# Kernel tuning notes

Hardware: AMD Instinct MI355X
Metric: run time of the kernel (lower is better)

Reference implementation:

```python
import jax, jax.numpy as jnp
import numpy as np

NUM_HEADS = 16
D_MODEL = 1024
DEPTH = D_MODEL // NUM_HEADS
THRESHOLD = 0.1
BATCH = 2
SEQ = 2048


def setup_inputs() -> dict:
    key = jax.random.key(0)
    ks = jax.random.split(key, 9)
    w_scale = 1.0 / np.sqrt(D_MODEL)
    Q = jax.random.normal(ks[0], (BATCH, SEQ, D_MODEL), dtype=jnp.float32)
    T = jax.random.normal(ks[1], (BATCH, SEQ, D_MODEL), dtype=jnp.float32)
    V = jax.random.normal(ks[2], (BATCH, SEQ, D_MODEL), dtype=jnp.float32)
    Wq = jax.random.normal(ks[3], (NUM_HEADS, D_MODEL, DEPTH), dtype=jnp.float32) * w_scale
    Wk = jax.random.normal(ks[4], (NUM_HEADS, D_MODEL, DEPTH), dtype=jnp.float32) * w_scale
    Wv = jax.random.normal(ks[5], (NUM_HEADS, D_MODEL, DEPTH), dtype=jnp.float32) * w_scale
    Wo = jax.random.normal(ks[6], (D_MODEL, D_MODEL), dtype=jnp.float32) * w_scale
    bq = jnp.zeros((NUM_HEADS, DEPTH), dtype=jnp.float32)
    bk = jnp.zeros((NUM_HEADS, DEPTH), dtype=jnp.float32)
    bv = jnp.zeros((NUM_HEADS, DEPTH), dtype=jnp.float32)
    bo = jnp.zeros((D_MODEL,), dtype=jnp.float32)
    return {"Q": Q, "T": T, "V": V, "Wq": Wq, "bq": bq, "Wk": Wk, "bk": bk,
            "Wv": Wv, "bv": bv, "Wo": Wo, "bo": bo}


def reference(Q, T, V, Wq, bq, Wk, bk, Wv, bv, Wo, bo):
    # Per-head projections (stacked over heads): [B,S,D] x [H,D,E] -> [B,H,S,E]
    q = jnp.einsum('bsd,hde->bhse', Q, Wq) + bq[None, :, None, :]
    k = jnp.einsum('bsd,hde->bhse', T, Wk) + bk[None, :, None, :]
    v = jnp.einsum('bsd,hde->bhse', V, Wv) + bv[None, :, None, :]

    # Raw scores (NOT pre-scaled): [B,H,S,S]
    scores = jnp.einsum('bhqe,bhke->bhqk', q, k)
    # tf.where(A>thr, A, -2**32 * cast(A>thr)) -> failing entries become 0
    scores = jnp.where(scores > THRESHOLD, scores, jnp.zeros((), scores.dtype))
    # M = 1 - lower_band(ones): +1 on strictly upper-triangular entries
    seq = scores.shape[-1]
    upper = jnp.triu(jnp.ones((seq, seq), dtype=scores.dtype), k=1)
    scores = (scores + upper) / jnp.sqrt(jnp.asarray(DEPTH, scores.dtype))

    attn = jax.nn.softmax(scores, axis=-1)
    out = jnp.einsum('bhqk,bhke->bhqe', attn, v)  # [B,H,S,E]
    B, H, S, E = out.shape
    concat = out.transpose(0, 2, 1, 3).reshape(B, S, H * E)  # [B,S,D]
    return concat @ Wo + bo
```

## Files before the change

### kernel.cpp

```cpp
#include <hip/hip_runtime.h>
#include <stdint.h>


typedef __attribute__((ext_vector_type(8))) short bf16x8;
typedef __attribute__((ext_vector_type(4))) float f32x4;

#define DEVFN static __device__ __forceinline__

static constexpr int S_ = 2048;
static constexpr int H_ = 16;

DEVFN unsigned short f2bf(float x) {
  union { float f; uint32_t u; } v; v.f = x;
  const uint32_t r = v.u + 0x7fffu + ((v.u >> 16) & 1u);
  return (unsigned short)(r >> 16);
}

DEVFN f32x4 fzero() { f32x4 v = {0.f, 0.f, 0.f, 0.f}; return v; }

DEVFN void gld_lds16(const void* g, void* lds) {
  __builtin_amdgcn_global_load_lds(
      (const __attribute__((address_space(1))) void*)g,
      (__attribute__((address_space(3))) void*)lds, 16, 0, 0);
}

__global__ void prep_weights(const float* __restrict__ Wq, const float* __restrict__ Wk,
                             const float* __restrict__ Wv, const float* __restrict__ Wo,
                             unsigned short* __restrict__ dstBase) {
  const int z = blockIdx.z;
  const float* src = (z == 0) ? Wq : (z == 1) ? Wk : (z == 2) ? Wv : Wo;
  unsigned short* dst = dstBase + (size_t)z * (1024u * 1024u);
  const int idx = blockIdx.x * 256 + threadIdx.x;
  const int c = idx & 1023;
  const int d0 = (idx >> 10) << 3;
  unsigned short hv[8];
#pragma unroll
  for (int t = 0; t < 8; ++t) {
    const int d = d0 + t;
    const float v = (z < 3) ? src[(size_t)((c >> 6) * 1024 + d) * 64 + (c & 63)]
                            : src[(size_t)d * 1024 + c];
    hv[t] = f2bf(v);
  }
  *(uint4*)(dst + (size_t)c * 1024 + d0) = *(const uint4*)hv;
}

__global__ void convert_a(const float* __restrict__ Qm, const float* __restrict__ Tm,
                          const float* __restrict__ Vm, unsigned short* __restrict__ aq,
                          unsigned short* __restrict__ at2, unsigned short* __restrict__ av) {
  const int z = blockIdx.z;
  const float* s = (z == 0) ? Qm : (z == 1) ? Tm : Vm;
  unsigned short* d = (z == 0) ? aq : (z == 1) ? at2 : av;
  const size_t i = ((size_t)blockIdx.x * 256 + threadIdx.x) * 8;
  const float4 f0 = *(const float4*)(s + i);
  const float4 f1 = *(const float4*)(s + i + 4);
  uint32_t d0, d1, d2, d3;
  asm("v_cvt_pk_bf16_f32 %0, %1, %2" : "=v"(d0) : "v"(f0.x), "v"(f0.y));
  asm("v_cvt_pk_bf16_f32 %0, %1, %2" : "=v"(d1) : "v"(f0.z), "v"(f0.w));
  asm("v_cvt_pk_bf16_f32 %0, %1, %2" : "=v"(d2) : "v"(f1.x), "v"(f1.y));
  asm("v_cvt_pk_bf16_f32 %0, %1, %2" : "=v"(d3) : "v"(f1.z), "v"(f1.w));
  uint4 o; o.x = d0; o.y = d1; o.z = d2; o.w = d3;
  *(uint4*)(d + i) = o;
}

__global__ __launch_bounds__(256, 4)
void proj_gemm(const unsigned short* __restrict__ Aq,
               const unsigned short* __restrict__ At2,
               const unsigned short* __restrict__ Av,
               const unsigned short* __restrict__ Wt,
               const float* __restrict__ bq, const float* __restrict__ bk,
               const float* __restrict__ bv, unsigned short* __restrict__ qb,
               unsigned short* __restrict__ kb, unsigned short* __restrict__ vtb) {
  __shared__ unsigned short At[2][128 * 32];
  __shared__ unsigned short Bt[2][128 * 32];

  const int tid = threadIdx.x;
  const int lane = tid & 63;
  const int w = tid >> 6;
  const int g = lane >> 4, c = lane & 15;
  const int wm = w >> 1, wn = w & 1;

  const int m0 = blockIdx.x * 128;
  const int proj = blockIdx.y >> 3;
  const int n0 = (blockIdx.y & 7) * 128;

  const unsigned short* Abf = (proj == 0) ? Aq : (proj == 1) ? At2 : Av;
  const unsigned short* W = Wt + (size_t)proj * (1024u * 1024u);

  f32x4 acc[4][4];
#pragma unroll
  for (int i = 0; i < 4; ++i)
#pragma unroll
    for (int j = 0; j < 4; ++j) acc[i][j] = fzero();

  const int srow = lane >> 2;
  const int sch = lane & 3;

  auto stage = [&](int kt, int buf) {
#pragma unroll
    for (int u = 0; u < 2; ++u) {
      const int row = u * 64 + w * 16 + srow;
      const int ch = sch ^ ((row >> 1) & 3);
      gld_lds16(Abf + (size_t)(m0 + row) * 1024 + kt * 32 + ch * 8,
                &At[buf][(u * 64 + w * 16) * 32]);
      gld_lds16(W + (size_t)(n0 + row) * 1024 + kt * 32 + ch * 8,
                &Bt[buf][(u * 64 + w * 16) * 32]);
    }
  };

  stage(0, 0);
  __syncthreads();

  for (int kt = 0; kt < 32; ++kt) {
    const int buf = kt & 1;
    if (kt < 31) stage(kt + 1, buf ^ 1);

    bf16x8 af[4], bfr[4];
#pragma unroll
    for (int mi = 0; mi < 4; ++mi) {
      const int row = wm * 64 + mi * 16 + c;
      af[mi] = *(const bf16x8*)&At[buf][row * 32 + ((g ^ ((row >> 1) & 3))) * 8];
    }
#pragma unroll
    for (int ni = 0; ni < 4; ++ni) {
      const int row = wn * 64 + ni * 16 + c;
      bfr[ni] = *(const bf16x8*)&Bt[buf][row * 32 + ((g ^ ((row >> 1) & 3))) * 8];
    }
#pragma unroll
    for (int mi = 0; mi < 4; ++mi)
#pragma unroll
      for (int ni = 0; ni < 4; ++ni)
        acc[mi][ni] = __builtin_amdgcn_mfma_f32_16x16x32_bf16(af[mi], bfr[ni],
                                                              acc[mi][ni], 0, 0, 0);
    __syncthreads();
  }

  const float* bias = (proj == 0) ? bq : (proj == 1) ? bk : bv;
#pragma unroll
  for (int ni = 0; ni < 4; ++ni) {
    const int colb = n0 + wn * 64 + ni * 16 + c;
    const float bc = bias[colb];
    const int hh = colb >> 6, e = colb & 63;
#pragma unroll
    for (int mi = 0; mi < 4; ++mi) {
#pragma unroll
      for (int r = 0; r < 4; ++r) {
        const int row = m0 + wm * 64 + mi * 16 + g * 4 + r;
        const int bb = row >> 11, s = row & 2047;
        const float val = acc[mi][ni][r] + bc;
        if (proj < 2) {
          unsigned short* d = (proj == 0) ? qb : kb;
          d[(((size_t)(bb * H_ + hh)) * S_ + s) * 64 + e] = f2bf(val);
        } else {
          vtb[(((size_t)(bb * H_ + hh)) * 64 + e) * S_ + s] = f2bf(val);
        }
      }
    }
  }
}

__global__ __launch_bounds__(256, 4)
void attn_kernel(const unsigned short* __restrict__ qb,
                 const unsigned short* __restrict__ kb,
                 const unsigned short* __restrict__ vtb,
                 unsigned short* __restrict__ att) {
  __shared__ unsigned short Kt[2][64 * 64];
  __shared__ unsigned short Vt[2][64 * 64];
  __shared__ unsigned short Pt[4][16 * 64];

  const int tid = threadIdx.x;
  const int lane = tid & 63;
  const int w = tid >> 6;
  const int g = lane >> 4, c = lane & 15;

  const int orig = blockIdx.x;
  const int logical = ((orig & 7) << 7) | (orig >> 3);
  const int qblk = logical & 31;
  const int bh = logical >> 5;
  const int hh = bh & 15, bz = bh >> 4;

  const int q0w = qblk * 64 + w * 16;
  const unsigned short* qh = qb + (size_t)bh * S_ * 64;
  const unsigned short* kh = kb + (size_t)bh * S_ * 64;
  const unsigned short* vh = vtb + (size_t)bh * 64 * S_;

  bf16x8 aq[2];
#pragma unroll
  for (int t = 0; t < 2; ++t)
    aq[t] = *(const bf16x8*)&qh[(size_t)(q0w + c) * 64 + t * 32 + g * 8];

  f32x4 O[4];
#pragma unroll
  for (int ne = 0; ne < 4; ++ne) O[ne] = fzero();
  float l_lane = 0.f;

  constexpr float L2E = 1.4426950408889634f;
  const float S2 = 0.125f * L2E;
  const float B2 = 0.125f * L2E;
  const int iq = q0w + c;

  const int srow = w * 8 + (lane >> 3);
  const int sch = lane & 7;

  {
#pragma unroll
    for (int u = 0; u < 2; ++u) {
      const int row = u * 32 + srow;
      gld_lds16(kh + (size_t)row * 64 + (sch ^ (row & 7)) * 8,
                &Kt[0][(u * 32 + w * 8) * 64]);
      gld_lds16(vh + (size_t)row * S_ + (sch ^ (row & 7)) * 8,
                &Vt[0][(u * 32 + w * 8) * 64]);
    }
  }
  __syncthreads();

  for (int jt = 0; jt < 32; ++jt) {
    const int cur = jt & 1;
    const int j0 = jt * 64;

    if (jt < 31) {
      const int jn = j0 + 64;
#pragma unroll
      for (int u = 0; u < 2; ++u) {
        const int row = u * 32 + srow;
        gld_lds16(kh + (size_t)(jn + row) * 64 + (sch ^ (row & 7)) * 8,
                  &Kt[cur ^ 1][(u * 32 + w * 8) * 64]);
        gld_lds16(vh + (size_t)row * S_ + jn + (sch ^ (row & 7)) * 8,
                  &Vt[cur ^ 1][(u * 32 + w * 8) * 64]);
      }
    }

    f32x4 sa[4];
#pragma unroll
    for (int mi = 0; mi < 4; ++mi) sa[mi] = fzero();
    __builtin_amdgcn_s_setprio(1);
#pragma unroll
    for (int ks = 0; ks < 2; ++ks) {
#pragma unroll
      for (int mi = 0; mi < 4; ++mi) {
        const int row = mi * 16 + c;
        const bf16x8 ka =
            *(const bf16x8*)&Kt[cur][row * 64 + ((ks * 4 + g) ^ (row & 7)) * 8];
        sa[mi] = __builtin_amdgcn_mfma_f32_16x16x32_bf16(ka, aq[ks], sa[mi], 0, 0, 0);
      }
    }
    __builtin_amdgcn_s_setprio(0);

    float pe[16];
    const bool allUp = (j0 >= q0w + 16);
    const bool noneUp = (j0 + 63 <= q0w);
    if (allUp || noneUp) {
      const float bb = allUp ? B2 : 0.f;
#pragma unroll
      for (int i = 0; i < 16; ++i) {
        const float v = sa[i >> 2][i & 3];
        const float arg = (v > 0.1f) ? __builtin_fmaf(v, S2, bb) : bb;
        pe[i] = __builtin_amdgcn_exp2f(arg);
      }
    } else {
#pragma unroll
      for (int mi = 0; mi < 4; ++mi)
#pragma unroll
        for (int r = 0; r < 4; ++r) {
          const float v = sa[mi][r];
          const float bb = (j0 + mi * 16 + g * 4 + r > iq) ? B2 : 0.f;
          const float arg = (v > 0.1f) ? __builtin_fmaf(v, S2, bb) : bb;
          pe[mi * 4 + r] = __builtin_amdgcn_exp2f(arg);
        }
    }

    {
      float s01 = pe[0] + pe[1], s23 = pe[2] + pe[3];
      float s45 = pe[4] + pe[5], s67 = pe[6] + pe[7];
      float s89 = pe[8] + pe[9], sab = pe[10] + pe[11];
      float scd = pe[12] + pe[13], sef = pe[14] + pe[15];
      l_lane += ((s01 + s23) + (s45 + s67)) + ((s89 + sab) + (scd + sef));
    }

#pragma unroll
    for (int mi = 0; mi < 4; ++mi) {
      uint2 d;
      asm("v_cvt_pk_bf16_f32 %0, %1, %2"
          : "=v"(d.x) : "v"(pe[mi * 4 + 0]), "v"(pe[mi * 4 + 1]));
      asm("v_cvt_pk_bf16_f32 %0, %1, %2"
          : "=v"(d.y) : "v"(pe[mi * 4 + 2]), "v"(pe[mi * 4 + 3]));
      const int pc = (2 * mi + (g >> 1)) ^ (c & 7);
      *(uint2*)&Pt[w][c * 64 + pc * 8 + (g & 1) * 4] = d;
    }
    asm volatile("s_waitcnt lgkmcnt(0)" ::: "memory");
    __builtin_amdgcn_sched_barrier(0);

    __builtin_amdgcn_s_setprio(1);
#pragma unroll
    for (int ks = 0; ks < 2; ++ks) {
      const bf16x8 pa =
          *(const bf16x8*)&Pt[w][c * 64 + (((ks * 4 + g) ^ (c & 7))) * 8];
#pragma unroll
      for (int ne = 0; ne < 4; ++ne) {
        const int e = ne * 16 + c;
        const bf16x8 bv8 =
            *(const bf16x8*)&Vt[cur][e * 64 + ((ks * 4 + g) ^ (e & 7)) * 8];
        O[ne] = __builtin_amdgcn_mfma_f32_16x16x32_bf16(pa, bv8, O[ne], 0, 0, 0);
      }
    }
    __builtin_amdgcn_s_setprio(0);
    __syncthreads();
  }

  float l = l_lane;
  l += __shfl_xor(l, 16);
  l += __shfl_xor(l, 32);
  const float invl = 1.f / l;
  const int base = (lane >> 2) & 12;
  float il[4];
#pragma unroll
  for (int r = 0; r < 4; ++r) il[r] = __shfl(invl, base + r);
#pragma unroll
  for (int r = 0; r < 4; ++r) {
    const int qg = q0w + g * 4 + r;
    const size_t ro = ((size_t)(bz * S_ + qg)) * 1024 + hh * 64;
#pragma unroll
    for (int ne = 0; ne < 4; ++ne)
      att[ro + ne * 16 + c] = f2bf(O[ne][r] * il[r]);
  }
}

__global__ __launch_bounds__(256, 3)
void out_gemm(const unsigned short* __restrict__ att,
              const unsigned short* __restrict__ WoT,
              const float* __restrict__ bo, float* __restrict__ outp) {
  __shared__ unsigned short At[2][128 * 32];
  __shared__ unsigned short Bt[2][128 * 32];

  const int tid = threadIdx.x;
  const int lane = tid & 63;
  const int w = tid >> 6;
  const int g = lane >> 4, c = lane & 15;
  const int wm = w >> 1, wn = w & 1;
  const int m0 = blockIdx.x * 128;
  const int n0 = blockIdx.y * 128;

  f32x4 acc[4][4];
#pragma unroll
  for (int i = 0; i < 4; ++i)
#pragma unroll
    for (int j = 0; j < 4; ++j) acc[i][j] = fzero();

  const int srow = lane >> 2;
  const int sch = lane & 3;

  auto stage = [&](int kt, int buf) {
#pragma unroll
    for (int u = 0; u < 2; ++u) {
      const int row = u * 64 + w * 16 + srow;
      const int ch = sch ^ ((row >> 1) & 3);
      gld_lds16(att + (size_t)(m0 + row) * 1024 + kt * 32 + ch * 8,
                &At[buf][(u * 64 + w * 16) * 32]);
      gld_lds16(WoT + (size_t)(n0 + row) * 1024 + kt * 32 + ch * 8,
                &Bt[buf][(u * 64 + w * 16) * 32]);
    }
  };

  stage(0, 0);
  __syncthreads();

  for (int kt = 0; kt < 32; ++kt) {
    const int buf = kt & 1;
    if (kt < 31) stage(kt + 1, buf ^ 1);

    bf16x8 af[4], bfr[4];
#pragma unroll
    for (int mi = 0; mi < 4; ++mi) {
      const int row = wm * 64 + mi * 16 + c;
      af[mi] = *(const bf16x8*)&At[buf][row * 32 + ((g ^ ((row >> 1) & 3))) * 8];
    }
#pragma unroll
    for (int ni = 0; ni < 4; ++ni) {
      const int row = wn * 64 + ni * 16 + c;
      bfr[ni] = *(const bf16x8*)&Bt[buf][row * 32 + ((g ^ ((row >> 1) & 3))) * 8];
    }
#pragma unroll
    for (int mi = 0; mi < 4; ++mi)
#pragma unroll
      for (int ni = 0; ni < 4; ++ni)
        acc[mi][ni] = __builtin_amdgcn_mfma_f32_16x16x32_bf16(af[mi], bfr[ni],
                                                              acc[mi][ni], 0, 0, 0);
    __syncthreads();
  }

#pragma unroll
  for (int ni = 0; ni < 4; ++ni) {
    const int colb = n0 + wn * 64 + ni * 16 + c;
    const float bc = bo[colb];
#pragma unroll
    for (int mi = 0; mi < 4; ++mi)
#pragma unroll
      for (int r = 0; r < 4; ++r) {
        const int row = m0 + wm * 64 + mi * 16 + g * 4 + r;
        outp[(size_t)row * 1024 + colb] = acc[mi][ni][r] + bc;
      }
  }
}

extern "C" void kernel_launch(void* const* d_in, const int* in_sizes, int n_in,
                              void* d_out, int out_size, void* d_ws, size_t ws_size,
                              hipStream_t stream) {
  const float* Q  = (const float*)d_in[0];
  const float* T  = (const float*)d_in[1];
  const float* V  = (const float*)d_in[2];
  const float* Wq = (const float*)d_in[3];
  const float* bq = (const float*)d_in[4];
  const float* Wk = (const float*)d_in[5];
  const float* bk = (const float*)d_in[6];
  const float* Wv = (const float*)d_in[7];
  const float* bv = (const float*)d_in[8];
  const float* Wo = (const float*)d_in[9];
  const float* bo = (const float*)d_in[10];

  const size_t MB = 1024ull * 1024ull;
  if (ws_size < 40 * MB) return;

  uint8_t* ws = (uint8_t*)d_ws;
  unsigned short* Wt  = (unsigned short*)(ws);
  unsigned short* qb  = (unsigned short*)(ws + 8 * MB);
  unsigned short* kb  = (unsigned short*)(ws + 16 * MB);
  unsigned short* vtb = (unsigned short*)(ws + 24 * MB);
  unsigned short* attb = (unsigned short*)(ws + 32 * MB);

  unsigned short* aQ = (unsigned short*)d_out;
  unsigned short* aT = aQ + 4ull * 1024ull * 1024ull;
  unsigned short* aV = attb;

  prep_weights<<<dim3(512, 1, 4), 256, 0, stream>>>(Wq, Wk, Wv, Wo, Wt);
  convert_a<<<dim3(2048, 1, 3), 256, 0, stream>>>(Q, T, V, aQ, aT, aV);
  proj_gemm<<<dim3(32, 24), 256, 0, stream>>>(aQ, aT, aV, Wt, bq, bk, bv,
                                              qb, kb, vtb);
  attn_kernel<<<dim3(1024), 256, 0, stream>>>(qb, kb, vtb, attb);
  out_gemm<<<dim3(32, 8), 256, 0, stream>>>(attb, Wt + 3ull * 1024ull * 1024ull,
                                            bo, (float*)d_out);
}
```

Before: 146.4 us.

## Compute softmax denominator via MFMA with ones, precompute LDS offsets, unroll tile loop

The attention kernel now computes the softmax row sum with an extra MFMA against a ones vector on the bf16 probabilities. This replaces the per-lane float accumulation and the shuffle reduction, so the denominator now comes from bf16-rounded values, matching what the PV product uses. LDS read/write offsets and global source pointers are precomputed outside the loop, and the tile loop is manually unrolled by two so the buffer index is a compile-time constant. The V projection epilogue also packs four bf16 values into one 8-byte store, replacing scalar strided stores.

Measured after the change: 138.1 us. -5.6%, faster.

```diff
diff --git a/kernel.cpp b/kernel.cpp
--- a/kernel.cpp
+++ b/kernel.cpp
@@ -135,24 +135,38 @@
   }
 
   const float* bias = (proj == 0) ? bq : (proj == 1) ? bk : bv;
-#pragma unroll
-  for (int ni = 0; ni < 4; ++ni) {
-    const int colb = n0 + wn * 64 + ni * 16 + c;
-    const float bc = bias[colb];
-    const int hh = colb >> 6, e = colb & 63;
-#pragma unroll
-    for (int mi = 0; mi < 4; ++mi) {
-#pragma unroll
-      for (int r = 0; r < 4; ++r) {
-        const int row = m0 + wm * 64 + mi * 16 + g * 4 + r;
-        const int bb = row >> 11, s = row & 2047;
-        const float val = acc[mi][ni][r] + bc;
-        if (proj < 2) {
-          unsigned short* d = (proj == 0) ? qb : kb;
-          d[(((size_t)(bb * H_ + hh)) * S_ + s) * 64 + e] = f2bf(val);
-        } else {
-          vtb[(((size_t)(bb * H_ + hh)) * 64 + e) * S_ + s] = f2bf(val);
+  if (proj < 2) {
+    unsigned short* dptr = (proj == 0) ? qb : kb;
+#pragma unroll
+    for (int ni = 0; ni < 4; ++ni) {
+      const int colb = n0 + wn * 64 + ni * 16 + c;
+      const float bc = bias[colb];
+      const int hh = colb >> 6, e = colb & 63;
+#pragma unroll
+      for (int mi = 0; mi < 4; ++mi)
+#pragma unroll
+        for (int r = 0; r < 4; ++r) {
+          const int row = m0 + wm * 64 + mi * 16 + g * 4 + r;
+          const int bb = row >> 11, s = row & 2047;
+          dptr[(((size_t)(bb * H_ + hh)) * S_ + s) * 64 + e] = f2bf(acc[mi][ni][r] + bc);
         }
+    }
+  } else {
+#pragma unroll
+    for (int ni = 0; ni < 4; ++ni) {
+      const int colb = n0 + wn * 64 + ni * 16 + c;
+      const float bc = bias[colb];
+      const int hh = colb >> 6, e = colb & 63;
+#pragma unroll
+      for (int mi = 0; mi < 4; ++mi) {
+        const int rowb = m0 + wm * 64 + mi * 16 + g * 4;
+        const int bb = rowb >> 11, s0 = rowb & 2047;
+        const float v0 = acc[mi][ni][0] + bc, v1 = acc[mi][ni][1] + bc;
+        const float v2 = acc[mi][ni][2] + bc, v3 = acc[mi][ni][3] + bc;
+        uint2 pk;
+        asm("v_cvt_pk_bf16_f32 %0, %1, %2" : "=v"(pk.x) : "v"(v0), "v"(v1));
+        asm("v_cvt_pk_bf16_f32 %0, %1, %2" : "=v"(pk.y) : "v"(v2), "v"(v3));
+        *(uint2*)&vtb[(((size_t)(bb * H_ + hh)) * 64 + e) * S_ + s0] = pk;
       }
     }
   }
@@ -188,139 +202,142 @@
   for (int t = 0; t < 2; ++t)
     aq[t] = *(const bf16x8*)&qh[(size_t)(q0w + c) * 64 + t * 32 + g * 8];
 
+  bf16x8 onesB;
+#pragma unroll
+  for (int i = 0; i < 8; ++i) onesB[i] = (short)0x3F80;
+
   f32x4 O[4];
+  f32x4 accL;
 #pragma unroll
   for (int ne = 0; ne < 4; ++ne) O[ne] = fzero();
-  float l_lane = 0.f;
+  accL = fzero();
 
   constexpr float L2E = 1.4426950408889634f;
   const float S2 = 0.125f * L2E;
   const float B2 = 0.125f * L2E;
   const int iq = q0w + c;
 
+  int kaOff[2][4], bvOff[2][4], paOff[2], pwOff[4];
+#pragma unroll
+  for (int ks = 0; ks < 2; ++ks) {
+#pragma unroll
+    for (int mi = 0; mi < 4; ++mi) {
+      const int row = mi * 16 + c;
+      kaOff[ks][mi] = 2 * (row * 64 + ((ks * 4 + g) ^ (row & 7)) * 8);
+    }
+#pragma unroll
+    for (int ne = 0; ne < 4; ++ne) {
+      const int e = ne * 16 + c;
+      bvOff[ks][ne] = 2 * (e * 64 + ((ks * 4 + g) ^ (e & 7)) * 8);
+    }
+    paOff[ks] = 2 * (c * 64 + ((ks * 4 + g) ^ (c & 7)) * 8);
+  }
+#pragma unroll
+  for (int mi = 0; mi < 4; ++mi)
+    pwOff[mi] = 2 * (c * 64 + ((2 * mi + (g >> 1)) ^ (c & 7)) * 8 + (g & 1) * 4);
+
   const int srow = w * 8 + (lane >> 3);
-  const int sch = lane & 7;
+  const int sch = (lane & 7) ^ (srow & 7);
+  const unsigned short* kS0 = kh + (size_t)srow * 64 + sch * 8;
+  const unsigned short* kS1 = kh + (size_t)(32 + srow) * 64 + sch * 8;
+  const unsigned short* vS0 = vh + (size_t)srow * S_ + sch * 8;
+  const unsigned short* vS1 = vh + (size_t)(32 + srow) * S_ + sch * 8;
 
   {
-#pragma unroll
-    for (int u = 0; u < 2; ++u) {
-      const int row = u * 32 + srow;
-      gld_lds16(kh + (size_t)row * 64 + (sch ^ (row & 7)) * 8,
-                &Kt[0][(u * 32 + w * 8) * 64]);
-      gld_lds16(vh + (size_t)row * S_ + (sch ^ (row & 7)) * 8,
-                &Vt[0][(u * 32 + w * 8) * 64]);
-    }
+    gld_lds16(kS0, &Kt[0][(w * 8) * 64]);
+    gld_lds16(kS1, &Kt[0][(32 + w * 8) * 64]);
+    gld_lds16(vS0, &Vt[0][(w * 8) * 64]);
+    gld_lds16(vS1, &Vt[0][(32 + w * 8) * 64]);
   }
   __syncthreads();
 
-  for (int jt = 0; jt < 32; ++jt) {
-    const int cur = jt & 1;
-    const int j0 = jt * 64;
-
-    if (jt < 31) {
-      const int jn = j0 + 64;
-#pragma unroll
-      for (int u = 0; u < 2; ++u) {
-        const int row = u * 32 + srow;
-        gld_lds16(kh + (size_t)(jn + row) * 64 + (sch ^ (row & 7)) * 8,
-                  &Kt[cur ^ 1][(u * 32 + w * 8) * 64]);
-        gld_lds16(vh + (size_t)row * S_ + jn + (sch ^ (row & 7)) * 8,
-                  &Vt[cur ^ 1][(u * 32 + w * 8) * 64]);
-      }
-    }
-
-    f32x4 sa[4];
-#pragma unroll
-    for (int mi = 0; mi < 4; ++mi) sa[mi] = fzero();
-    __builtin_amdgcn_s_setprio(1);
-#pragma unroll
-    for (int ks = 0; ks < 2; ++ks) {
-#pragma unroll
-      for (int mi = 0; mi < 4; ++mi) {
-        const int row = mi * 16 + c;
-        const bf16x8 ka =
-            *(const bf16x8*)&Kt[cur][row * 64 + ((ks * 4 + g) ^ (row & 7)) * 8];
-        sa[mi] = __builtin_amdgcn_mfma_f32_16x16x32_bf16(ka, aq[ks], sa[mi], 0, 0, 0);
-      }
-    }
-    __builtin_amdgcn_s_setprio(0);
-
-    float pe[16];
-    const bool allUp = (j0 >= q0w + 16);
-    const bool noneUp = (j0 + 63 <= q0w);
-    if (allUp || noneUp) {
-      const float bb = allUp ? B2 : 0.f;
-#pragma unroll
-      for (int i = 0; i < 16; ++i) {
-        const float v = sa[i >> 2][i & 3];
-        const float arg = (v > 0.1f) ? __builtin_fmaf(v, S2, bb) : bb;
-        pe[i] = __builtin_amdgcn_exp2f(arg);
-      }
-    } else {
-#pragma unroll
-      for (int mi = 0; mi < 4; ++mi)
-#pragma unroll
-        for (int r = 0; r < 4; ++r) {
-          const float v = sa[mi][r];
-          const float bb = (j0 + mi * 16 + g * 4 + r > iq) ? B2 : 0.f;
-          const float arg = (v > 0.1f) ? __builtin_fmaf(v, S2, bb) : bb;
-          pe[mi * 4 + r] = __builtin_amdgcn_exp2f(arg);
-        }
-    }
-
-    {
-      float s01 = pe[0] + pe[1], s23 = pe[2] + pe[3];
-      float s45 = pe[4] + pe[5], s67 = pe[6] + pe[7];
-      float s89 = pe[8] + pe[9], sab = pe[10] + pe[11];
-      float scd = pe[12] + pe[13], sef = pe[14] + pe[15];
-      l_lane += ((s01 + s23) + (s45 + s67)) + ((s89 + sab) + (scd + sef));
-    }
-
-#pragma unroll
-    for (int mi = 0; mi < 4; ++mi) {
-      uint2 d;
-      asm("v_cvt_pk_bf16_f32 %0, %1, %2"
-          : "=v"(d.x) : "v"(pe[mi * 4 + 0]), "v"(pe[mi * 4 + 1]));
-      asm("v_cvt_pk_bf16_f32 %0, %1, %2"
-          : "=v"(d.y) : "v"(pe[mi * 4 + 2]), "v"(pe[mi * 4 + 3]));
-      const int pc = (2 * mi + (g >> 1)) ^ (c & 7);
-      *(uint2*)&Pt[w][c * 64 + pc * 8 + (g & 1) * 4] = d;
-    }
-    asm volatile("s_waitcnt lgkmcnt(0)" ::: "memory");
-    __builtin_amdgcn_sched_barrier(0);
-
-    __builtin_amdgcn_s_setprio(1);
-#pragma unroll
-    for (int ks = 0; ks < 2; ++ks) {
-      const bf16x8 pa =
-          *(const bf16x8*)&Pt[w][c * 64 + (((ks * 4 + g) ^ (c & 7))) * 8];
-#pragma unroll
-      for (int ne = 0; ne < 4; ++ne) {
-        const int e = ne * 16 + c;
-        const bf16x8 bv8 =
-            *(const bf16x8*)&Vt[cur][e * 64 + ((ks * 4 + g) ^ (e & 7)) * 8];
-        O[ne] = __builtin_amdgcn_mfma_f32_16x16x32_bf16(pa, bv8, O[ne], 0, 0, 0);
-      }
-    }
-    __builtin_amdgcn_s_setprio(0);
-    __syncthreads();
-  }
-
-  float l = l_lane;
-  l += __shfl_xor(l, 16);
-  l += __shfl_xor(l, 32);
-  const float invl = 1.f / l;
-  const int base = (lane >> 2) & 12;
-  float il[4];
-#pragma unroll
-  for (int r = 0; r < 4; ++r) il[r] = __shfl(invl, base + r);
+#define ATTN_BODY(JT, CUR)                                                     \
+  do {                                                                         \
+    const int j0 = (JT) * 64;                                                  \
+    if ((JT) < 31) {             \
+      gld_lds16(kS0 + 4096, &Kt[CUR ^ 1][(w * 8) * 64]);                       \
+      gld_lds16(kS1 + 4096, &Kt[CUR ^ 1][(32 + w * 8) * 64]);                  \
+      gld_lds16(vS0 + 64, &Vt[CUR ^ 1][(w * 8) * 64]);                         \
+      gld_lds16(vS1 + 64, &Vt[CUR ^ 1][(32 + w * 8) * 64]);                    \
+      kS0 += 4096; kS1 += 4096; vS0 += 64; vS1 += 64;                          \
+    }                                                                          \
+    f32x4 sa[4];                                                               \
+    _Pragma("unroll")                                                          \
+    for (int mi = 0; mi < 4; ++mi) sa[mi] = fzero();                           \
+    __builtin_amdgcn_s_setprio(1);                                             \
+    _Pragma("unroll")                                                          \
+    for (int ks = 0; ks < 2; ++ks)                                             \
+      _Pragma("unroll")                                                        \
+      for (int mi = 0; mi < 4; ++mi) {                                         \
+        const bf16x8 ka =                                                      \
+            *(const bf16x8*)((const char*)&Kt[CUR][0] + kaOff[ks][mi]);        \
+        sa[mi] = __builtin_amdgcn_mfma_f32_16x16x32_bf16(ka, aq[ks], sa[mi],   \
+                                                         0, 0, 0);             \
+      }                                                                        \
+    __builtin_amdgcn_s_setprio(0);                                             \
+    const bool allUp = (j0 >= q0w + 16);                                       \
+    const bool noneUp = (j0 + 63 <= q0w);                                      \
+    _Pragma("unroll")                                                          \
+    for (int mi = 0; mi < 4; ++mi) {                                           \
+      float pv[4];                                                             \
+      if (allUp || noneUp) {                                                   \
+        const float bb = allUp ? B2 : 0.f;                                     \
+        _Pragma("unroll")                                                      \
+        for (int r = 0; r < 4; ++r) {                                          \
+          const float v = sa[mi][r];                                           \
+          pv[r] = __builtin_amdgcn_exp2f((v > 0.1f)                            \
+                                             ? __builtin_fmaf(v, S2, bb)      \
+                                             : bb);                            \
+        }                                                                      \
+      } else {                                                                 \
+        _Pragma("unroll")                                                      \
+        for (int r = 0; r < 4; ++r) {                                          \
+          const float v = sa[mi][r];                                           \
+          const float bb = (j0 + mi * 16 + g * 4 + r > iq) ? B2 : 0.f;         \
+          pv[r] = __builtin_amdgcn_exp2f((v > 0.1f)                            \
+                                             ? __builtin_fmaf(v, S2, bb)      \
+                                             : bb);                           \
+        }                                                                      \
+      }                                                                        \
+      uint2 d;                                                                 \
+      asm("v_cvt_pk_bf16_f32 %0, %1, %2" : "=v"(d.x) : "v"(pv[0]), "v"(pv[1]));\
+      asm("v_cvt_pk_bf16_f32 %0, %1, %2" : "=v"(d.y) : "v"(pv[2]), "v"(pv[3]));\
+      *(uint2*)((char*)&Pt[w][0] + pwOff[mi]) = d;                             \
+    }                                                                          \
+    asm volatile("s_waitcnt lgkmcnt(0)" ::: "memory");                         \
+    __builtin_amdgcn_sched_barrier(0);                                         \
+    __builtin_amdgcn_s_setprio(1);                                             \
+    _Pragma("unroll")                                                          \
+    for (int ks = 0; ks < 2; ++ks) {                                           \
+      const bf16x8 pa =                                                        \
+          *(const bf16x8*)((const char*)&Pt[w][0] + paOff[ks]);                \
+      accL = __builtin_amdgcn_mfma_f32_16x16x32_bf16(pa, onesB, accL, 0, 0, 0);\
+      _Pragma("unroll")                                                        \
+      for (int ne = 0; ne < 4; ++ne) {                                         \
+        const bf16x8 bv8 =                                                     \
+            *(const bf16x8*)((const char*)&Vt[CUR][0] + bvOff[ks][ne]);        \
+        O[ne] = __builtin_amdgcn_mfma_f32_16x16x32_bf16(pa, bv8, O[ne],        \
+                                                        0, 0, 0);              \
+      }                                                                        \
+    }                                                                          \
+    __builtin_amdgcn_s_setprio(0);                                             \
+    __syncthreads();                                                           \
+  } while (0)
+
+  for (int jt = 0; jt < 32; jt += 2) {
+    ATTN_BODY(jt, 0);
+    ATTN_BODY(jt + 1, 1);
+  }
+#undef ATTN_BODY
+
 #pragma unroll
   for (int r = 0; r < 4; ++r) {
+    const float il = 1.f / accL[r];
     const int qg = q0w + g * 4 + r;
     const size_t ro = ((size_t)(bz * S_ + qg)) * 1024 + hh * 64;
 #pragma unroll
     for (int ne = 0; ne < 4; ++ne)
-      att[ro + ne * 16 + c] = f2bf(O[ne][r] * il[r]);
+      att[ro + ne * 16 + c] = f2bf(O[ne][r] * il);
   }
 }
 
```
